# Kernel tuning notes

Hardware: AMD Instinct MI355X
Metric: run time of the kernel (lower is better)

## Reference

```python
import jax, jax.numpy as jnp
import numpy as np

EPS = 1e-5
NEG = -1000000000.0

def _layernorm(x, g, b):
    m = x.mean(-1, keepdims=True)
    v = ((x - m) ** 2).mean(-1, keepdims=True)
    return (x - m) / jnp.sqrt(v + EPS) * g + b

D_MODEL, N_HEADS, D_K, D_V, D_FF = 768, 12, 64, 64, 3072
VOCAB, MAX_POS, N_LAYERS = 32000, 2048, 2
B, S = 2, 2048

def setup_inputs() -> dict:
    key = jax.random.key(0)
    ks = jax.random.split(key, 16)
    sc = 0.02
    L = N_LAYERS
    return {
        "inputs": jax.random.randint(ks[0], (B, S), 0, VOCAB, dtype=jnp.int64) if jax.config.jax_enable_x64 else jax.random.randint(ks[0], (B, S), 0, VOCAB, dtype=jnp.int32),
        "attention_mask": jax.random.randint(ks[1], (B, S), 0, 2, dtype=jnp.int32),
        "emb": jax.random.normal(ks[2], (VOCAB, D_MODEL), jnp.float32) * sc,
        "pos_emb": jax.random.normal(ks[3], (MAX_POS, D_MODEL), jnp.float32) * sc,
        "wq": jax.random.normal(ks[4], (L, D_MODEL, N_HEADS * D_K), jnp.float32) * sc,
        "wk": jax.random.normal(ks[5], (L, D_MODEL, N_HEADS * D_K), jnp.float32) * sc,
        "wv": jax.random.normal(ks[6], (L, D_MODEL, N_HEADS * D_V), jnp.float32) * sc,
        "wo": jax.random.normal(ks[7], (L, N_HEADS * D_V, D_MODEL), jnp.float32) * sc,
        "ln1_g": jnp.ones((L, D_MODEL), jnp.float32),
        "ln1_b": jnp.zeros((L, D_MODEL), jnp.float32),
        "w1": jax.random.normal(ks[8], (L, D_MODEL, D_FF), jnp.float32) * sc,
        "b1": jnp.zeros((L, D_FF), jnp.float32),
        "w2": jax.random.normal(ks[9], (L, D_FF, D_MODEL), jnp.float32) * sc,
        "b2": jnp.zeros((L, D_MODEL), jnp.float32),
        "ln2_g": jnp.ones((L, D_MODEL), jnp.float32),
        "ln2_b": jnp.zeros((L, D_MODEL), jnp.float32),
    }

def reference(inputs, attention_mask, emb, pos_emb, wq, wk, wv, wo,
              ln1_g, ln1_b, w1, b1, w2, b2, ln2_g, ln2_b):
    b, s = inputs.shape
    x = emb[inputs] + pos_emb[jnp.arange(s)][None, :, :]  # [B,S,D]
    # combined mask: True where pad token OR strictly-upper (future) position
    sub = jnp.triu(jnp.ones((s, s), dtype=bool), k=1)            # [S,S]
    pad = (attention_mask == 0)[:, None, :]                      # [B,1,S]
    mask = (pad | sub[None, :, :])[:, None, :, :]                # [B,1,S,S] -> broadcast over heads
    # FAITHFUL to source: masked_fill(attention_mask == 0, -1e9) fills where mask is FALSE
    scale = 1.0 / float(np.sqrt(D_K))
    attns = []
    for l in range(N_LAYERS):
        q = (x @ wq[l]).reshape(b, s, N_HEADS, D_K).transpose(0, 2, 1, 3)  # [B,H,S,dk]
        k = (x @ wk[l]).reshape(b, s, N_HEADS, D_K).transpose(0, 2, 1, 3)
        v = (x @ wv[l]).reshape(b, s, N_HEADS, D_V).transpose(0, 2, 1, 3)
        scores = jnp.einsum('bhqd,bhkd->bhqk', q, k) * scale
        scores = jnp.where(mask, scores, NEG)  # fill -1e9 where mask == False (as in source)
        attn = jax.nn.softmax(scores, axis=-1)
        ctx = jnp.einsum('bhqk,bhkd->bhqd', attn, v)
        ctx = ctx.transpose(0, 2, 1, 3).reshape(b, s, N_HEADS * D_V)
        x = _layernorm(ctx @ wo[l] + x, ln1_g[l], ln1_b[l])
        ff = jnp.maximum(x @ w1[l] + b1[l], 0.0) @ w2[l] + b2[l]
        x = _layernorm(ff + x, ln2_g[l], ln2_b[l])
        attns.append(attn)
    return x, jnp.stack(attns)  # [B,S,D], [L,B,H,S,S]
```

## Files before the change

kernel.cpp:

```cpp
#include <hip/hip_runtime.h>
#include <math.h>

#define DM 768
#define NH 12
#define DK 64
#define DFF 3072
#define BB 2
#define SS 2048
#define NL 2

typedef __attribute__((ext_vector_type(8))) short short8;
typedef __attribute__((ext_vector_type(4))) float f32x4;

__device__ inline unsigned short f2bf(float f) {
    unsigned int u = __float_as_uint(f);
    u += 0x7fffu + ((u >> 16) & 1u);
    return (unsigned short)(u >> 16);
}
__device__ inline float bf2f(unsigned short h) {
    return __uint_as_float(((unsigned int)h) << 16);
}

#define GL16(g, l) __builtin_amdgcn_global_load_lds( \
    (const __attribute__((address_space(1))) void*)(g), \
    (__attribute__((address_space(3))) void*)(l), 16, 0, 0)

__global__ __launch_bounds__(256) void embed_kernel(
    const int* __restrict__ toks, const float* __restrict__ emb,
    const float* __restrict__ pos, float* __restrict__ x,
    unsigned short* __restrict__ xb)
{
    int rs = blockIdx.x;
    int s = rs & (SS - 1);
    int tok = toks[rs];
    int t = threadIdx.x;
    const float* e = emb + (size_t)tok * DM;
    const float* p = pos + (size_t)s * DM;
    float* xr = x + (size_t)rs * DM;
    unsigned short* xbr = xb + (size_t)rs * DM;
#pragma unroll
    for (int i = 0; i < 3; ++i) {
        int c = t + 256 * i;
        float v = e[c] + p[c];
        xr[c] = v;
        xbr[c] = f2bf(v);
    }
}

__global__ __launch_bounds__(256) void prep_weights(
    const float* __restrict__ wq, const float* __restrict__ wk,
    const float* __restrict__ wv, const float* __restrict__ wo,
    const float* __restrict__ w1, const float* __restrict__ w2,
    unsigned short* __restrict__ wt)
{
    __shared__ float tile[32][33];
    int id = blockIdx.x;
    int l = id / 6912; id -= l * 6912;
    unsigned short* wtl = wt + (size_t)l * 7077888;
    const float* src; unsigned short* dst; int Kd, Nd, nt, kt;
    if (id < 2304) {
        int m = id / 576, r = id % 576;
        src = ((m == 0) ? wq : (m == 1) ? wk : (m == 2) ? wv : wo) + (size_t)l * DM * DM;
        dst = wtl + (size_t)m * 589824;
        Kd = 768; Nd = 768; nt = r / 24; kt = r % 24;
    } else if (id < 4608) {
        int r = id - 2304;
        src = w1 + (size_t)l * DM * DFF; dst = wtl + 2359296; Kd = 768; Nd = 3072;
        nt = r / 24; kt = r % 24;
    } else {
        int r = id - 4608;
        src = w2 + (size_t)l * DFF * DM; dst = wtl + 4718592; Kd = 3072; Nd = 768;
        nt = r / 96; kt = r % 96;
    }
    int n0 = nt * 32, k0 = kt * 32;
    int c = threadIdx.x & 31, rr = threadIdx.x >> 5;
#pragma unroll
    for (int i = 0; i < 32; i += 8)
        tile[rr + i][c] = src[(size_t)(k0 + rr + i) * Nd + n0 + c];
    __syncthreads();
#pragma unroll
    for (int i = 0; i < 32; i += 8)
        dst[(size_t)(n0 + rr + i) * Kd + k0 + c] = f2bf(tile[c][rr + i]);
}

__global__ __launch_bounds__(256) void transpose_v(
    const unsigned short* __restrict__ vb, unsigned short* __restrict__ vt)
{
    __shared__ unsigned short tile[32][33];
    int c0 = blockIdx.x * 32;
    int r0 = blockIdx.y * 32;
    int c = threadIdx.x & 31, rr = threadIdx.x >> 5;
#pragma unroll
    for (int i = 0; i < 32; i += 8)
        tile[rr + i][c] = vb[(size_t)(r0 + rr + i) * DM + c0 + c];
    __syncthreads();
    int b = r0 >> 11;
    int s0 = r0 & 2047;
#pragma unroll
    for (int i = 0; i < 32; i += 8)
        vt[((size_t)b * DM + c0 + rr + i) * SS + s0 + c] = tile[c][rr + i];
}

template<int OUT_MODE>
__global__ __launch_bounds__(256) void gemm_bt(
    const unsigned short* __restrict__ A, const unsigned short* __restrict__ Bt,
    const float* __restrict__ bias, void* __restrict__ Cv,
    int K, int lda, int ldb, int ldc)
{
    __shared__ unsigned short As[128 * 32];
    __shared__ unsigned short Bs[128 * 32];
    const int t = threadIdx.x;
    const int row0 = blockIdx.y * 128;
    const int col0 = blockIdx.x * 128;
    const int z = (OUT_MODE == 0) ? blockIdx.z : 0;
    if (OUT_MODE == 0) { A += (size_t)z * K; Bt += (size_t)z * K; }
    const int lane = t & 63, wid = t >> 6;
    const int wr = wid >> 1, wc = wid & 1;
    const int half = lane >> 4, lr = lane & 15;
    f32x4 acc[4][4] = {};

    const int o = t * 16;
    const int srow = o >> 6;
    const int skb = (o & 63) >> 1;

    for (int k0 = 0; k0 < K; k0 += 32) {
        GL16(A + (size_t)(row0 + srow) * lda + k0 + skb, (unsigned short*)As + o / 2);
        GL16(A + (size_t)(row0 + 64 + srow) * lda + k0 + skb, (unsigned short*)As + 2048 + o / 2);
        GL16(Bt + (size_t)(col0 + srow) * ldb + k0 + skb, (unsigned short*)Bs + o / 2);
        GL16(Bt + (size_t)(col0 + 64 + srow) * ldb + k0 + skb, (unsigned short*)Bs + 2048 + o / 2);
        __syncthreads();
        short8 af[4], bfr[4];
#pragma unroll
        for (int m = 0; m < 4; ++m)
            af[m] = *(const short8*)&As[(wr * 64 + m * 16 + lr) * 32 + half * 8];
#pragma unroll
        for (int n = 0; n < 4; ++n)
            bfr[n] = *(const short8*)&Bs[(wc * 64 + n * 16 + lr) * 32 + half * 8];
#pragma unroll
        for (int m = 0; m < 4; ++m)
#pragma unroll
            for (int n = 0; n < 4; ++n)
                acc[m][n] = __builtin_amdgcn_mfma_f32_16x16x32_bf16(af[m], bfr[n], acc[m][n], 0, 0, 0);
        __syncthreads();
    }

#pragma unroll
    for (int m = 0; m < 4; ++m) {
#pragma unroll
        for (int n = 0; n < 4; ++n) {
            const int cidx = col0 + wc * 64 + n * 16 + lr;
            const float bv = bias ? bias[cidx] : 0.0f;
#pragma unroll
            for (int j = 0; j < 4; ++j) {
                const int r = row0 + wr * 64 + m * 16 + half * 4 + j;
                float v = acc[m][n][j] + bv;
                if (OUT_MODE == 2) v = fmaxf(v, 0.0f);
                if (OUT_MODE == 0) {
                    ((float*)Cv)[((size_t)z * 4096 + r) * ldc + cidx] = v;
                } else if (OUT_MODE == 4) {
                    int mi = (cidx >= 1536) ? 2 : (cidx >= 768 ? 1 : 0);
                    int cl = cidx - mi * 768;
                    ((unsigned short*)Cv)[((size_t)mi * 4096 + r) * 768 + cl] = f2bf(v);
                } else {
                    ((unsigned short*)Cv)[(size_t)r * ldc + cidx] = f2bf(v);
                }
            }
        }
    }
}

__global__ __launch_bounds__(256) void attn_fused(
    const unsigned short* __restrict__ qg, const unsigned short* __restrict__ kg,
    const unsigned short* __restrict__ vt, const int* __restrict__ amask,
    float* __restrict__ attnL, unsigned short* __restrict__ cb)
{
    __shared__ unsigned short Ks[2][128 * 64];
    __shared__ unsigned short Vs[2][64 * 128];
    __shared__ unsigned short Es[32 * 128];
    __shared__ float redsum[4][32];
    __shared__ float invs[32];

    const int t = threadIdx.x;
    const int id = blockIdx.x;
    const int xcd = id & 7, idx = id >> 3;
    const int bh = xcd * 3 + (idx >> 6);
    const int qt = idx & 63;
    const int b = bh / NH, h = bh % NH;
    const int q0 = qt * 32;
    const int lane = t & 63, w = t >> 6;
    const int half = lane >> 4, lr = lane & 15;
    const int* am = amask + b * SS;

    const unsigned short* qbase = qg + ((size_t)b * SS + q0 + lr) * DM + h * DK + half * 8;
    short8 afq[2][2];
    afq[0][0] = *(const short8*)(qbase);
    afq[0][1] = *(const short8*)(qbase + 32);
    afq[1][0] = *(const short8*)(qbase + 16 * DM);
    afq[1][1] = *(const short8*)(qbase + 16 * DM + 32);

    const unsigned short* Kg = kg + (size_t)b * SS * DM + h * DK;
    const unsigned short* Vg = vt + ((size_t)b * DM + h * DK) * SS;

#define STAGE_K(kt, buf) { \
    _Pragma("unroll") \
    for (int r_ = 0; r_ < 4; ++r_) { \
        int o_ = r_ * 4096 + t * 16; \
        int krow_ = o_ >> 7; \
        int cp_ = (o_ >> 4) & 7; \
        GL16(Kg + (size_t)((kt) * 128 + krow_) * DM + ((cp_ ^ (krow_ & 7)) << 3), (char*)Ks[buf] + o_); \
    } }
#define STAGE_V(kt, buf) { \
    _Pragma("unroll") \
    for (int r_ = 0; r_ < 4; ++r_) { \
        int o_ = r_ * 4096 + t * 16; \
        int d_ = o_ >> 8; \
        int cp_ = (o_ >> 4) & 15; \
        GL16(Vg + (size_t)d_ * SS + (kt) * 128 + ((cp_ ^ (d_ & 7)) << 3), (char*)Vs[buf] + o_); \
    } }

    float vsum[2][4] = {};
    STAGE_K(0, 0);
    for (int kt = 0; kt < 16; ++kt) {
        asm volatile("s_waitcnt vmcnt(0)" ::: "memory");
        __builtin_amdgcn_s_barrier();
        if (kt < 15) STAGE_K(kt + 1, (kt + 1) & 1);
        const char* kbuf = (const char*)Ks[kt & 1];
#pragma unroll
        for (int nn = 0; nn < 2; ++nn) {
            const int krl = w * 32 + nn * 16 + lr;
            const char* kr = kbuf + krl * 128;
            const int ksw = krl & 7;
            short8 bk0 = *(const short8*)(kr + ((half ^ ksw) << 4));
            short8 bk1 = *(const short8*)(kr + (((4 + half) ^ ksw) << 4));
            const int kpos = kt * 128 + krl;
            const bool pad = (am[kpos] == 0);
#pragma unroll
            for (int m = 0; m < 2; ++m) {
                f32x4 s = {};
                s = __builtin_amdgcn_mfma_f32_16x16x32_bf16(afq[m][0], bk0, s, 0, 0, 0);
                s = __builtin_amdgcn_mfma_f32_16x16x32_bf16(afq[m][1], bk1, s, 0, 0, 0);
#pragma unroll
                for (int j = 0; j < 4; ++j) {
                    int qpos = q0 + m * 16 + half * 4 + j;
                    if (pad || (kpos > qpos))
                        vsum[m][j] += __expf(0.125f * s[j]);
                }
            }
        }
    }
    __syncthreads();

#pragma unroll
    for (int m = 0; m < 2; ++m)
#pragma unroll
        for (int j = 0; j < 4; ++j) {
            vsum[m][j] += __shfl_xor(vsum[m][j], 1, 64);
            vsum[m][j] += __shfl_xor(vsum[m][j], 2, 64);
            vsum[m][j] += __shfl_xor(vsum[m][j], 4, 64);
            vsum[m][j] += __shfl_xor(vsum[m][j], 8, 64);
        }
    if (lr == 0) {
#pragma unroll
        for (int m = 0; m < 2; ++m)
#pragma unroll
            for (int j = 0; j < 4; ++j)
                redsum[w][m * 16 + half * 4 + j] = vsum[m][j];
    }
    __syncthreads();
    if (t < 32) {
        float rs = redsum[0][t] + redsum[1][t] + redsum[2][t] + redsum[3][t];
        invs[t] = (rs > 0.0f) ? 1.0f / rs : 0.0f;
    }
    __syncthreads();

    f32x4 ctxa[2] = {};
    float* ab = attnL + ((size_t)bh * SS + q0) * SS;
    STAGE_K(0, 0);
    STAGE_V(0, 0);
    for (int kt = 0; kt < 16; ++kt) {
        if (kt == 0) {
            asm volatile("s_waitcnt vmcnt(0)" ::: "memory");
        } else {
            asm volatile("s_waitcnt vmcnt(4)" ::: "memory");
        }
        __builtin_amdgcn_s_barrier();
        if (kt < 15) { STAGE_K(kt + 1, (kt + 1) & 1); STAGE_V(kt + 1, (kt + 1) & 1); }
        const char* kbuf = (const char*)Ks[kt & 1];
#pragma unroll
        for (int nn = 0; nn < 2; ++nn) {
            const int krl = w * 32 + nn * 16 + lr;
            const char* kr = kbuf + krl * 128;
            const int ksw = krl & 7;
            short8 bk0 = *(const short8*)(kr + ((half ^ ksw) << 4));
            short8 bk1 = *(const short8*)(kr + (((4 + half) ^ ksw) << 4));
            const int kpos = kt * 128 + krl;
            const bool pad = (am[kpos] == 0);
#pragma unroll
            for (int m = 0; m < 2; ++m) {
                f32x4 s = {};
                s = __builtin_amdgcn_mfma_f32_16x16x32_bf16(afq[m][0], bk0, s, 0, 0, 0);
                s = __builtin_amdgcn_mfma_f32_16x16x32_bf16(afq[m][1], bk1, s, 0, 0, 0);
#pragma unroll
                for (int j = 0; j < 4; ++j) {
                    int row = m * 16 + half * 4 + j;
                    int qpos = q0 + row;
                    bool keep = pad || (kpos > qpos);
                    float e = keep ? __expf(0.125f * s[j]) * invs[row] : 0.0f;
                    *((unsigned short*)((char*)Es + row * 256 + ((krl * 2) ^ ((row & 7) << 4)))) = f2bf(e);
                }
            }
        }
        asm volatile("s_waitcnt lgkmcnt(0)" ::: "memory");
        __builtin_amdgcn_s_barrier();

        const char* vbuf = (const char*)Vs[kt & 1];
#pragma unroll
        for (int ks = 0; ks < 4; ++ks) {
            const int dl = w * 16 + lr;
            const int cv = ks * 4 + half;
            short8 bv = *(const short8*)(vbuf + dl * 256 + ((cv ^ (dl & 7)) << 4));
#pragma unroll
            for (int m = 0; m < 2; ++m) {
                short8 ae = *(const short8*)((const char*)Es + (m * 16 + lr) * 256 +
                                             ((ks * 64 + half * 16) ^ ((lr & 7) << 4)));
                ctxa[m] = __builtin_amdgcn_mfma_f32_16x16x32_bf16(ae, bv, ctxa[m], 0, 0, 0);
            }
        }

        {
            const int prow = t >> 3, pchunk = t & 7;
            const char* erow = (const char*)Es + prow * 256;
            const int swz = (prow & 7) << 4;
            short8 e0 = *(const short8*)(erow + ((pchunk * 32) ^ swz));
            short8 e1 = *(const short8*)(erow + ((pchunk * 32 + 16) ^ swz));
            float* dst = ab + (size_t)prow * SS + kt * 128 + pchunk * 16;
            f32x4 o0, o1, o2, o3;
            o0[0] = bf2f((unsigned short)e0[0]); o0[1] = bf2f((unsigned short)e0[1]);
            o0[2] = bf2f((unsigned short)e0[2]); o0[3] = bf2f((unsigned short)e0[3]);
            o1[0] = bf2f((unsigned short)e0[4]); o1[1] = bf2f((unsigned short)e0[5]);
            o1[2] = bf2f((unsigned short)e0[6]); o1[3] = bf2f((unsigned short)e0[7]);
            o2[0] = bf2f((unsigned short)e1[0]); o2[1] = bf2f((unsigned short)e1[1]);
            o2[2] = bf2f((unsigned short)e1[2]); o2[3] = bf2f((unsigned short)e1[3]);
            o3[0] = bf2f((unsigned short)e1[4]); o3[1] = bf2f((unsigned short)e1[5]);
            o3[2] = bf2f((unsigned short)e1[6]); o3[3] = bf2f((unsigned short)e1[7]);
            __builtin_nontemporal_store(o0, (f32x4*)dst);
            __builtin_nontemporal_store(o1, (f32x4*)(dst + 4));
            __builtin_nontemporal_store(o2, (f32x4*)(dst + 8));
            __builtin_nontemporal_store(o3, (f32x4*)(dst + 12));
        }
    }

#pragma unroll
    for (int m = 0; m < 2; ++m)
#pragma unroll
        for (int j = 0; j < 4; ++j) {
            int row = m * 16 + half * 4 + j;
            cb[((size_t)b * SS + q0 + row) * DM + h * DK + w * 16 + lr] = f2bf(ctxa[m][j]);
        }
#undef STAGE_K
#undef STAGE_V
}

__global__ __launch_bounds__(256) void add_ln_kernel(
    const float* __restrict__ p0, const float* __restrict__ p1,
    const float* __restrict__ bias, const float* __restrict__ xin,
    const float* __restrict__ g, const float* __restrict__ bta,
    float* __restrict__ xout, unsigned short* __restrict__ xbout)
{
    int row = blockIdx.x;
    int t = threadIdx.x;
    const float* a0 = p0 + (size_t)row * DM;
    const float* a1 = p1 + (size_t)row * DM;
    const float* xr = xin + (size_t)row * DM;
    float* orow = xout + (size_t)row * DM;
    unsigned short* obr = xbout + (size_t)row * DM;
    __shared__ float red[256];
    float v[3];
    float sum = 0.0f;
#pragma unroll
    for (int i = 0; i < 3; ++i) {
        int c = t + 256 * i;
        v[i] = a0[c] + a1[c] + xr[c] + (bias ? bias[c] : 0.0f);
        sum += v[i];
    }
    red[t] = sum;
    __syncthreads();
    for (int s = 128; s > 0; s >>= 1) {
        if (t < s) red[t] += red[t + s];
        __syncthreads();
    }
    float mean = red[0] * (1.0f / DM);
    __syncthreads();
    float sq = 0.0f;
#pragma unroll
    for (int i = 0; i < 3; ++i) {
        float d = v[i] - mean;
        sq += d * d;
    }
    red[t] = sq;
    __syncthreads();
    for (int s = 128; s > 0; s >>= 1) {
        if (t < s) red[t] += red[t + s];
        __syncthreads();
    }
    float inv = 1.0f / sqrtf(red[0] * (1.0f / DM) + 1e-5f);
#pragma unroll
    for (int i = 0; i < 3; ++i) {
        int c = t + 256 * i;
        float ov = (v[i] - mean) * inv * g[c] + bta[c];
        orow[c] = ov;
        obr[c] = f2bf(ov);
    }
}

extern "C" void kernel_launch(void* const* d_in, const int* in_sizes, int n_in,
                              void* d_out, int out_size, void* d_ws, size_t ws_size,
                              hipStream_t stream)
{
    const int*   toks  = (const int*)d_in[0];
    const int*   amask = (const int*)d_in[1];
    const float* emb   = (const float*)d_in[2];
    const float* pos   = (const float*)d_in[3];
    const float* wq    = (const float*)d_in[4];
    const float* wk    = (const float*)d_in[5];
    const float* wv    = (const float*)d_in[6];
    const float* wo    = (const float*)d_in[7];
    const float* ln1g  = (const float*)d_in[8];
    const float* ln1b  = (const float*)d_in[9];
    const float* w1    = (const float*)d_in[10];
    const float* b1    = (const float*)d_in[11];
    const float* w2    = (const float*)d_in[12];
    const float* b2    = (const float*)d_in[13];
    const float* ln2g  = (const float*)d_in[14];
    const float* ln2b  = (const float*)d_in[15];

    float* out = (float*)d_out;
    char*  wsb = (char*)d_ws;

    const size_t ROWS = (size_t)BB * SS;
    const size_t XSZ  = ROWS * DM;
    const size_t ATTN_L = (size_t)BB * NH * SS * SS;

    float*          x    = (float*)(wsb);
    unsigned short* xb   = (unsigned short*)(wsb + 12582912);
    unsigned short* qb   = (unsigned short*)(wsb + 18874368);
    unsigned short* kbuf = (unsigned short*)(wsb + 25165824);
    unsigned short* vb   = (unsigned short*)(wsb + 31457280);
    unsigned short* cb   = (unsigned short*)(wsb + 37748736);
    float*          p0   = (float*)(wsb + 44040192);
    float*          p1   = (float*)(wsb + 56623104);
    unsigned short* vt   = (unsigned short*)(wsb + 69206016);
    unsigned short* ffb  = (unsigned short*)(wsb + 69206016);
    unsigned short* wt   = (unsigned short*)(wsb + 94371840);

    float* attn_out = out + XSZ;

    embed_kernel<<<ROWS, 256, 0, stream>>>(toks, emb, pos, x, xb);
    prep_weights<<<13824, 256, 0, stream>>>(wq, wk, wv, wo, w1, w2, wt);

    for (int l = 0; l < NL; ++l) {
        unsigned short* QKVT = wt + (size_t)l * 7077888;
        unsigned short* WOT  = QKVT + 1769472;
        unsigned short* W1T  = QKVT + 2359296;
        unsigned short* W2T  = QKVT + 4718592;

        gemm_bt<4><<<dim3(18, 32), 256, 0, stream>>>(xb, QKVT, nullptr, qb, DM, DM, DM, DM);
        transpose_v<<<dim3(24, 128), 256, 0, stream>>>(vb, vt);

        float* attnL = attn_out + (size_t)l * ATTN_L;
        attn_fused<<<1536, 256, 0, stream>>>(qb, kbuf, vt, amask, attnL, cb);

        gemm_bt<0><<<dim3(6, 32, 2), 256, 0, stream>>>(cb, WOT, nullptr, p0, 384, DM, DM, DM);
        add_ln_kernel<<<ROWS, 256, 0, stream>>>(p0, p0 + XSZ, nullptr, x,
                                                ln1g + l * DM, ln1b + l * DM, x, xb);

        gemm_bt<2><<<dim3(24, 32), 256, 0, stream>>>(xb, W1T, b1 + (size_t)l * DFF, ffb, DM, DM, DM, DFF);
        gemm_bt<0><<<dim3(6, 32, 2), 256, 0, stream>>>(ffb, W2T, nullptr, p0, 1536, DFF, DFF, DM);

        float* xdst = (l == NL - 1) ? out : x;
        add_ln_kernel<<<ROWS, 256, 0, stream>>>(p0, p0 + XSZ, b2 + (size_t)l * DM, x,
                                                ln2g + l * DM, ln2b + l * DM, xdst, xb);
    }
    (void)p1;
}
```

Before: 875.0 us.

## Double GEMM K-tile with swizzled LDS and use 64-row query tiles in attention

The GEMM now stages 64-wide K slices per iteration with an XOR-swizzled LDS layout, which halves the number of barrier pairs and is meant to avoid bank conflicts on fragment reads. The attention kernel processes 64 query rows per block instead of 32, so each K/V tile staged from global memory is reused across twice as many queries. The launch shrinks to 768 blocks. The reduction scratch is folded into the enlarged Es buffer, and the first K/V prefetch for the second pass is issued before the row-sum reduction. The larger tiles raise register and LDS use and may lower occupancy.

New measurement: 1.798 ms. +105.5%, slower.

```diff
diff --git a/kernel.cpp b/kernel.cpp
--- a/kernel.cpp
+++ b/kernel.cpp
@@ -107,8 +107,8 @@
     const float* __restrict__ bias, void* __restrict__ Cv,
     int K, int lda, int ldb, int ldc)
 {
-    __shared__ unsigned short As[128 * 32];
-    __shared__ unsigned short Bs[128 * 32];
+    __shared__ unsigned short As[128 * 64];
+    __shared__ unsigned short Bs[128 * 64];
     const int t = threadIdx.x;
     const int row0 = blockIdx.y * 128;
     const int col0 = blockIdx.x * 128;
@@ -119,28 +119,36 @@
     const int half = lane >> 4, lr = lane & 15;
     f32x4 acc[4][4] = {};
 
-    const int o = t * 16;
-    const int srow = o >> 6;
-    const int skb = (o & 63) >> 1;
-
-    for (int k0 = 0; k0 < K; k0 += 32) {
-        GL16(A + (size_t)(row0 + srow) * lda + k0 + skb, (unsigned short*)As + o / 2);
-        GL16(A + (size_t)(row0 + 64 + srow) * lda + k0 + skb, (unsigned short*)As + 2048 + o / 2);
-        GL16(Bt + (size_t)(col0 + srow) * ldb + k0 + skb, (unsigned short*)Bs + o / 2);
-        GL16(Bt + (size_t)(col0 + 64 + srow) * ldb + k0 + skb, (unsigned short*)Bs + 2048 + o / 2);
+    for (int k0 = 0; k0 < K; k0 += 64) {
+#pragma unroll
+        for (int r_ = 0; r_ < 4; ++r_) {
+            int o_ = r_ * 4096 + t * 16;
+            int row_ = o_ >> 7;
+            int cp_ = (o_ >> 4) & 7;
+            int gk_ = (cp_ ^ (row_ & 7)) << 3;
+            GL16(A + (size_t)(row0 + row_) * lda + k0 + gk_, (char*)As + o_);
+            GL16(Bt + (size_t)(col0 + row_) * ldb + k0 + gk_, (char*)Bs + o_);
+        }
         __syncthreads();
-        short8 af[4], bfr[4];
-#pragma unroll
-        for (int m = 0; m < 4; ++m)
-            af[m] = *(const short8*)&As[(wr * 64 + m * 16 + lr) * 32 + half * 8];
-#pragma unroll
-        for (int n = 0; n < 4; ++n)
-            bfr[n] = *(const short8*)&Bs[(wc * 64 + n * 16 + lr) * 32 + half * 8];
-#pragma unroll
-        for (int m = 0; m < 4; ++m)
-#pragma unroll
-            for (int n = 0; n < 4; ++n)
-                acc[m][n] = __builtin_amdgcn_mfma_f32_16x16x32_bf16(af[m], bfr[n], acc[m][n], 0, 0, 0);
+#pragma unroll
+        for (int kk = 0; kk < 2; ++kk) {
+            short8 a_[4], b_[4];
+#pragma unroll
+            for (int m = 0; m < 4; ++m) {
+                int row_ = wr * 64 + m * 16 + lr;
+                a_[m] = *(const short8*)&As[row_ * 64 + (((kk * 4 + half) ^ (row_ & 7)) << 3)];
+            }
+#pragma unroll
+            for (int n = 0; n < 4; ++n) {
+                int row_ = wc * 64 + n * 16 + lr;
+                b_[n] = *(const short8*)&Bs[row_ * 64 + (((kk * 4 + half) ^ (row_ & 7)) << 3)];
+            }
+#pragma unroll
+            for (int m = 0; m < 4; ++m)
+#pragma unroll
+                for (int n = 0; n < 4; ++n)
+                    acc[m][n] = __builtin_amdgcn_mfma_f32_16x16x32_bf16(a_[m], b_[n], acc[m][n], 0, 0, 0);
+        }
         __syncthreads();
     }
 
@@ -176,27 +184,26 @@
 {
     __shared__ unsigned short Ks[2][128 * 64];
     __shared__ unsigned short Vs[2][64 * 128];
-    __shared__ unsigned short Es[32 * 128];
-    __shared__ float redsum[4][32];
-    __shared__ float invs[32];
+    __shared__ unsigned short Es[64 * 128];
 
     const int t = threadIdx.x;
     const int id = blockIdx.x;
     const int xcd = id & 7, idx = id >> 3;
-    const int bh = xcd * 3 + (idx >> 6);
-    const int qt = idx & 63;
+    const int bh = xcd * 3 + (idx >> 5);
+    const int qt = idx & 31;
     const int b = bh / NH, h = bh % NH;
-    const int q0 = qt * 32;
+    const int q0 = qt * 64;
     const int lane = t & 63, w = t >> 6;
     const int half = lane >> 4, lr = lane & 15;
     const int* am = amask + b * SS;
 
     const unsigned short* qbase = qg + ((size_t)b * SS + q0 + lr) * DM + h * DK + half * 8;
-    short8 afq[2][2];
-    afq[0][0] = *(const short8*)(qbase);
-    afq[0][1] = *(const short8*)(qbase + 32);
-    afq[1][0] = *(const short8*)(qbase + 16 * DM);
-    afq[1][1] = *(const short8*)(qbase + 16 * DM + 32);
+    short8 afq[4][2];
+#pragma unroll
+    for (int m = 0; m < 4; ++m) {
+        afq[m][0] = *(const short8*)(qbase + m * 16 * DM);
+        afq[m][1] = *(const short8*)(qbase + m * 16 * DM + 32);
+    }
 
     const unsigned short* Kg = kg + (size_t)b * SS * DM + h * DK;
     const unsigned short* Vg = vt + ((size_t)b * DM + h * DK) * SS;
@@ -218,7 +225,7 @@
         GL16(Vg + (size_t)d_ * SS + (kt) * 128 + ((cp_ ^ (d_ & 7)) << 3), (char*)Vs[buf] + o_); \
     } }
 
-    float vsum[2][4] = {};
+    float vsum[4][4] = {};
     STAGE_K(0, 0);
     for (int kt = 0; kt < 16; ++kt) {
         asm volatile("s_waitcnt vmcnt(0)" ::: "memory");
@@ -235,7 +242,7 @@
             const int kpos = kt * 128 + krl;
             const bool pad = (am[kpos] == 0);
 #pragma unroll
-            for (int m = 0; m < 2; ++m) {
+            for (int m = 0; m < 4; ++m) {
                 f32x4 s = {};
                 s = __builtin_amdgcn_mfma_f32_16x16x32_bf16(afq[m][0], bk0, s, 0, 0, 0);
                 s = __builtin_amdgcn_mfma_f32_16x16x32_bf16(afq[m][1], bk1, s, 0, 0, 0);
@@ -248,10 +255,13 @@
             }
         }
     }
-    __syncthreads();
-
-#pragma unroll
-    for (int m = 0; m < 2; ++m)
+    STAGE_K(0, 0);
+    STAGE_V(0, 0);
+    __syncthreads();
+
+    float* red = (float*)Es;
+#pragma unroll
+    for (int m = 0; m < 4; ++m)
 #pragma unroll
         for (int j = 0; j < 4; ++j) {
             vsum[m][j] += __shfl_xor(vsum[m][j], 1, 64);
@@ -261,27 +271,32 @@
         }
     if (lr == 0) {
 #pragma unroll
-        for (int m = 0; m < 2; ++m)
+        for (int m = 0; m < 4; ++m)
 #pragma unroll
             for (int j = 0; j < 4; ++j)
-                redsum[w][m * 16 + half * 4 + j] = vsum[m][j];
-    }
-    __syncthreads();
-    if (t < 32) {
-        float rs = redsum[0][t] + redsum[1][t] + redsum[2][t] + redsum[3][t];
-        invs[t] = (rs > 0.0f) ? 1.0f / rs : 0.0f;
-    }
-    __syncthreads();
-
-    f32x4 ctxa[2] = {};
+                red[w * 64 + m * 16 + half * 4 + j] = vsum[m][j];
+    }
+    __syncthreads();
+    if (t < 64) {
+        float rs = red[t] + red[64 + t] + red[128 + t] + red[192 + t];
+        red[256 + t] = (rs > 0.0f) ? 1.0f / rs : 0.0f;
+    }
+    __syncthreads();
+    float rinv[4][4];
+#pragma unroll
+    for (int m = 0; m < 4; ++m)
+#pragma unroll
+        for (int j = 0; j < 4; ++j)
+            rinv[m][j] = red[256 + m * 16 + half * 4 + j];
+    __syncthreads();
+
+    f32x4 ctxa[4] = {};
     float* ab = attnL + ((size_t)bh * SS + q0) * SS;
-    STAGE_K(0, 0);
-    STAGE_V(0, 0);
     for (int kt = 0; kt < 16; ++kt) {
         if (kt == 0) {
             asm volatile("s_waitcnt vmcnt(0)" ::: "memory");
         } else {
-            asm volatile("s_waitcnt vmcnt(4)" ::: "memory");
+            asm volatile("s_waitcnt vmcnt(8)" ::: "memory");
         }
         __builtin_amdgcn_s_barrier();
         if (kt < 15) { STAGE_K(kt + 1, (kt + 1) & 1); STAGE_V(kt + 1, (kt + 1) & 1); }
@@ -296,7 +311,7 @@
             const int kpos = kt * 128 + krl;
             const bool pad = (am[kpos] == 0);
 #pragma unroll
-            for (int m = 0; m < 2; ++m) {
+            for (int m = 0; m < 4; ++m) {
                 f32x4 s = {};
                 s = __builtin_amdgcn_mfma_f32_16x16x32_bf16(afq[m][0], bk0, s, 0, 0, 0);
                 s = __builtin_amdgcn_mfma_f32_16x16x32_bf16(afq[m][1], bk1, s, 0, 0, 0);
@@ -305,7 +320,7 @@
                     int row = m * 16 + half * 4 + j;
                     int qpos = q0 + row;
                     bool keep = pad || (kpos > qpos);
-                    float e = keep ? __expf(0.125f * s[j]) * invs[row] : 0.0f;
+                    float e = keep ? __expf(0.125f * s[j]) * rinv[m][j] : 0.0f;
                     *((unsigned short*)((char*)Es + row * 256 + ((krl * 2) ^ ((row & 7) << 4)))) = f2bf(e);
                 }
             }
@@ -320,7 +335,7 @@
             const int cv = ks * 4 + half;
             short8 bv = *(const short8*)(vbuf + dl * 256 + ((cv ^ (dl & 7)) << 4));
 #pragma unroll
-            for (int m = 0; m < 2; ++m) {
+            for (int m = 0; m < 4; ++m) {
                 short8 ae = *(const short8*)((const char*)Es + (m * 16 + lr) * 256 +
                                              ((ks * 64 + half * 16) ^ ((lr & 7) << 4)));
                 ctxa[m] = __builtin_amdgcn_mfma_f32_16x16x32_bf16(ae, bv, ctxa[m], 0, 0, 0);
@@ -328,30 +343,28 @@
         }
 
         {
-            const int prow = t >> 3, pchunk = t & 7;
+            const int prow = t >> 2, pg = t & 3;
             const char* erow = (const char*)Es + prow * 256;
             const int swz = (prow & 7) << 4;
-            short8 e0 = *(const short8*)(erow + ((pchunk * 32) ^ swz));
-            short8 e1 = *(const short8*)(erow + ((pchunk * 32 + 16) ^ swz));
-            float* dst = ab + (size_t)prow * SS + kt * 128 + pchunk * 16;
-            f32x4 o0, o1, o2, o3;
-            o0[0] = bf2f((unsigned short)e0[0]); o0[1] = bf2f((unsigned short)e0[1]);
-            o0[2] = bf2f((unsigned short)e0[2]); o0[3] = bf2f((unsigned short)e0[3]);
-            o1[0] = bf2f((unsigned short)e0[4]); o1[1] = bf2f((unsigned short)e0[5]);
-            o1[2] = bf2f((unsigned short)e0[6]); o1[3] = bf2f((unsigned short)e0[7]);
-            o2[0] = bf2f((unsigned short)e1[0]); o2[1] = bf2f((unsigned short)e1[1]);
-            o2[2] = bf2f((unsigned short)e1[2]); o2[3] = bf2f((unsigned short)e1[3]);
-            o3[0] = bf2f((unsigned short)e1[4]); o3[1] = bf2f((unsigned short)e1[5]);
-            o3[2] = bf2f((unsigned short)e1[6]); o3[3] = bf2f((unsigned short)e1[7]);
-            __builtin_nontemporal_store(o0, (f32x4*)dst);
-            __builtin_nontemporal_store(o1, (f32x4*)(dst + 4));
-            __builtin_nontemporal_store(o2, (f32x4*)(dst + 8));
-            __builtin_nontemporal_store(o3, (f32x4*)(dst + 12));
-        }
-    }
-
-#pragma unroll
-    for (int m = 0; m < 2; ++m)
+            float* drow = ab + (size_t)prow * SS + kt * 128;
+#pragma unroll
+            for (int c = 0; c < 4; ++c) {
+                const int chunk = pg * 4 + c;
+                short8 ev = *(const short8*)(erow + ((chunk * 16) ^ swz));
+                float* dst = drow + chunk * 8;
+                f32x4 o0, o1;
+                o0[0] = bf2f((unsigned short)ev[0]); o0[1] = bf2f((unsigned short)ev[1]);
+                o0[2] = bf2f((unsigned short)ev[2]); o0[3] = bf2f((unsigned short)ev[3]);
+                o1[0] = bf2f((unsigned short)ev[4]); o1[1] = bf2f((unsigned short)ev[5]);
+                o1[2] = bf2f((unsigned short)ev[6]); o1[3] = bf2f((unsigned short)ev[7]);
+                __builtin_nontemporal_store(o0, (f32x4*)dst);
+                __builtin_nontemporal_store(o1, (f32x4*)(dst + 4));
+            }
+        }
+    }
+
+#pragma unroll
+    for (int m = 0; m < 4; ++m)
 #pragma unroll
         for (int j = 0; j < 4; ++j) {
             int row = m * 16 + half * 4 + j;
@@ -448,7 +461,6 @@
     unsigned short* vb   = (unsigned short*)(wsb + 31457280);
     unsigned short* cb   = (unsigned short*)(wsb + 37748736);
     float*          p0   = (float*)(wsb + 44040192);
-    float*          p1   = (float*)(wsb + 56623104);
     unsigned short* vt   = (unsigned short*)(wsb + 69206016);
     unsigned short* ffb  = (unsigned short*)(wsb + 69206016);
     unsigned short* wt   = (unsigned short*)(wsb + 94371840);
@@ -468,7 +480,7 @@
         transpose_v<<<dim3(24, 128), 256, 0, stream>>>(vb, vt);
 
         float* attnL = attn_out + (size_t)l * ATTN_L;
-        attn_fused<<<1536, 256, 0, stream>>>(qb, kbuf, vt, amask, attnL, cb);
+        attn_fused<<<768, 256, 0, stream>>>(qb, kbuf, vt, amask, attnL, cb);
 
         gemm_bt<0><<<dim3(6, 32, 2), 256, 0, stream>>>(cb, WOT, nullptr, p0, 384, DM, DM, DM);
         add_ln_kernel<<<ROWS, 256, 0, stream>>>(p0, p0 + XSZ, nullptr, x,
@@ -481,5 +493,4 @@
         add_ln_kernel<<<ROWS, 256, 0, stream>>>(p0, p0 + XSZ, b2 + (size_t)l * DM, x,
                                                 ln2g + l * DM, ln2b + l * DM, xdst, xb);
     }
-    (void)p1;
-}
+}
```
